# Kernel optimization log

Hardware: AMD Instinct MI355X
Metric: run time of the kernel (lower is better)

The kernel has to match this reference:

```python
import jax, jax.numpy as jnp
import numpy as np

N_QUBITS = 5
Q_DEPTH = 1
HALF_PI = np.pi / 2.0

H_GATE = (1.0 / np.sqrt(2.0)) * jnp.array([[1, 1], [1, -1]], dtype=jnp.complex64)
CNOT = jnp.array([[1, 0, 0, 0],
                  [0, 1, 0, 0],
                  [0, 0, 0, 1],
                  [0, 0, 1, 0]], dtype=jnp.complex64).reshape(2, 2, 2, 2)


def _apply_1q(state, gate, wire):
    # state: (2,)*N_QUBITS complex, gate: (2,2) complex
    state = jnp.tensordot(gate, state, axes=([1], [wire]))
    return jnp.moveaxis(state, 0, wire)


def _apply_cnot(state, control, target):
    state = jnp.tensordot(CNOT, state, axes=([2, 3], [control, target]))
    return jnp.moveaxis(state, (0, 1), (control, target))


def _ry(t):
    c = jnp.cos(t / 2).astype(jnp.complex64)
    s = jnp.sin(t / 2).astype(jnp.complex64)
    return jnp.stack([jnp.stack([c, -s]), jnp.stack([s, c])])


def _rx(t):
    c = jnp.cos(t / 2).astype(jnp.complex64)
    js = (-1j) * jnp.sin(t / 2).astype(jnp.complex64)
    return jnp.stack([jnp.stack([c, js]), jnp.stack([js, c])])


def _circuit(angles, q_weights):
    # angles: (N_QUBITS,), q_weights: (Q_DEPTH, N_QUBITS)
    state = jnp.zeros((2,) * N_QUBITS, dtype=jnp.complex64).at[(0,) * N_QUBITS].set(1.0)
    for w in range(N_QUBITS):
        state = _apply_1q(state, H_GATE, w)
    for w in range(N_QUBITS):
        state = _apply_1q(state, _ry(angles[w]), w)
    for k in range(Q_DEPTH):
        # BasicEntanglerLayers: RX rotations then ring of CNOTs
        for w in range(N_QUBITS):
            state = _apply_1q(state, _rx(q_weights[k, w]), w)
        for w in range(N_QUBITS):
            state = _apply_cnot(state, w, (w + 1) % N_QUBITS)
    probs = state.real ** 2 + state.imag ** 2
    zvals = []
    for w in range(N_QUBITS):
        p = probs.sum(axis=tuple(i for i in range(N_QUBITS) if i != w))  # (2,)
        zvals.append(p[0] - p[1])
    return jnp.stack(zvals)  # (N_QUBITS,)


def setup_inputs() -> dict:
    key = jax.random.key(0)
    k1, k2, k3, k4, k5, k6 = jax.random.split(key, 6)
    B = 65536
    return {
        "input_features": jax.random.normal(k1, (B, 512), dtype=jnp.float32),
        "w_pre": jax.random.normal(k2, (N_QUBITS, 512), dtype=jnp.float32) * 0.04,
        "b_pre": jax.random.normal(k3, (N_QUBITS,), dtype=jnp.float32) * 0.04,
        "q_params": 0.01 * jax.random.uniform(k4, (Q_DEPTH * N_QUBITS,), dtype=jnp.float32),
        "w_post": jax.random.normal(k5, (2, N_QUBITS), dtype=jnp.float32) * 0.4,
        "b_post": jax.random.normal(k6, (2,), dtype=jnp.float32) * 0.4,
    }


def reference(input_features, w_pre, b_pre, q_params, w_post, b_post):
    pre_out = input_features @ w_pre.T + b_pre            # (B, 5)
    q_in = jnp.tanh(pre_out) * HALF_PI                    # (B, 5)
    q_weights = q_params.reshape(Q_DEPTH, N_QUBITS)
    q_out = jax.vmap(lambda a: _circuit(a, q_weights))(q_in)  # (B, 5) real
    q_out = q_out.astype(jnp.float32)
    return q_out @ w_post.T + b_post                      # (B, 2)
```

## Files before the change

kernel.cpp:

```cpp
#include <hip/hip_runtime.h>
#include <math.h>

#define NQ 5
#define D 512
#define HALF_PI 1.57079632679489662f


__global__ __launch_bounds__(256) void dressed_qnet_kernel(
    const float* __restrict__ x,
    const float* __restrict__ w_pre,
    const float* __restrict__ b_pre,
    const float* __restrict__ q_params,
    const float* __restrict__ w_post,
    const float* __restrict__ b_post,
    float* __restrict__ out,
    int B)
{
    const int lane = threadIdx.x & 63;
    const int wave_in_block = threadIdx.x >> 6;
    const int waves_per_block = blockDim.x >> 6;
    const int wave_id = blockIdx.x * waves_per_block + wave_in_block;
    const int n_waves = gridDim.x * waves_per_block;

    float4 w0[NQ], w1[NQ];
#pragma unroll
    for (int q = 0; q < NQ; ++q) {
        w0[q] = *reinterpret_cast<const float4*>(w_pre + q * D + lane * 4);
        w1[q] = *reinterpret_cast<const float4*>(w_pre + q * D + 256 + lane * 4);
    }

    float bp[NQ], ct[NQ];
#pragma unroll
    for (int q = 0; q < NQ; ++q) {
        bp[q] = b_pre[q];
        ct[q] = __cosf(q_params[q]);
    }
    float wp0[NQ], wp1[NQ];
#pragma unroll
    for (int q = 0; q < NQ; ++q) {
        wp0[q] = w_post[q];
        wp1[q] = w_post[NQ + q];
    }
    const float bpost0 = b_post[0];
    const float bpost1 = b_post[1];

    for (int row = wave_id; row < B; row += n_waves) {
        const float4* xr = reinterpret_cast<const float4*>(x + (size_t)row * D);
        const float4 x0 = xr[lane];
        const float4 x1 = xr[lane + 64];

        float acc[NQ];
#pragma unroll
        for (int q = 0; q < NQ; ++q) {
            float s;
            s  = x0.x * w0[q].x;
            s  = fmaf(x0.y, w0[q].y, s);
            s  = fmaf(x0.z, w0[q].z, s);
            s  = fmaf(x0.w, w0[q].w, s);
            s  = fmaf(x1.x, w1[q].x, s);
            s  = fmaf(x1.y, w1[q].y, s);
            s  = fmaf(x1.z, w1[q].z, s);
            s  = fmaf(x1.w, w1[q].w, s);
            acc[q] = s;
        }

#pragma unroll
        for (int q = 0; q < NQ; ++q) {
            float v = acc[q];
#pragma unroll
            for (int off = 32; off >= 1; off >>= 1)
                v += __shfl_xor(v, off, 64);
            acc[q] = v;
        }

        float z[NQ];
#pragma unroll
        for (int q = 0; q < NQ; ++q) {
            const float p = acc[q] + bp[q];
            const float e = __expf(2.0f * p);
            const float th = 1.0f - 2.0f / (e + 1.0f);
            z[q] = -__sinf(HALF_PI * th) * ct[q];
        }

        const float v1   = z[0] * z[1];
        const float z234 = z[2] * z[3] * z[4];
        const float v0   = z[1] * z234;
        const float v2   = v1 * z[2];
        const float v3   = v2 * z[3];
        const float v4   = v1 * z234;

        float o0 = bpost0, o1 = bpost1;
        o0 = fmaf(wp0[0], v0, o0); o1 = fmaf(wp1[0], v0, o1);
        o0 = fmaf(wp0[1], v1, o0); o1 = fmaf(wp1[1], v1, o1);
        o0 = fmaf(wp0[2], v2, o0); o1 = fmaf(wp1[2], v2, o1);
        o0 = fmaf(wp0[3], v3, o0); o1 = fmaf(wp1[3], v3, o1);
        o0 = fmaf(wp0[4], v4, o0); o1 = fmaf(wp1[4], v4, o1);

        if (lane == 0) {
            reinterpret_cast<float2*>(out)[row] = make_float2(o0, o1);
        }
    }
}

extern "C" void kernel_launch(void* const* d_in, const int* in_sizes, int n_in,
                              void* d_out, int out_size, void* d_ws, size_t ws_size,
                              hipStream_t stream) {
    const float* x        = (const float*)d_in[0];
    const float* w_pre    = (const float*)d_in[1];
    const float* b_pre    = (const float*)d_in[2];
    const float* q_params = (const float*)d_in[3];
    const float* w_post   = (const float*)d_in[4];
    const float* b_post   = (const float*)d_in[5];
    float* out = (float*)d_out;

    const int B = in_sizes[0] / D;

    const int threads = 256;
    const int blocks = 2048;
    dressed_qnet_kernel<<<blocks, threads, 0, stream>>>(
        x, w_pre, b_pre, q_params, w_post, b_post, out, B);
}
```

Measured before the change: 33.07 us.

## Batch four rows per wave with upfront nontemporal loads and DPP wave reductions

Replaces the grid-stride row loop with a one-shot mapping in which each wave processes four rows. All of that wave's x loads are issued up front as nontemporal loads to raise memory-level parallelism. The shuffle-based wave reduction is replaced with DPP adds, a ds_swizzle and readlanes, and the four rows' outputs are written as two vector stores. The trade-off is more blocks and extra registers per wave, and the grid becomes fully sized to B.

```diff
diff --git a/kernel.cpp b/kernel.cpp
--- a/kernel.cpp
+++ b/kernel.cpp
@@ -3,8 +3,28 @@
 
 #define NQ 5
 #define D 512
+#define R 4
 #define HALF_PI 1.57079632679489662f
 
+typedef float f32x4 __attribute__((ext_vector_type(4)));
+
+
+#define DPP_ADD(v, CTRL)                                                        \
+    ((v) + __builtin_bit_cast(float, __builtin_amdgcn_update_dpp(               \
+               0, __builtin_bit_cast(int, (v)), (CTRL), 0xF, 0xF, true)))
+
+__device__ __forceinline__ float wave_sum(float v) {
+    v = DPP_ADD(v, 0xB1);
+    v = DPP_ADD(v, 0x4E);
+    v = DPP_ADD(v, 0x141);
+    v = DPP_ADD(v, 0x140);
+    int vi = __builtin_amdgcn_ds_swizzle(__builtin_bit_cast(int, v), 0x401F);
+    v = v + __builtin_bit_cast(float, vi);
+    const int vb = __builtin_bit_cast(int, v);
+    const float lo = __builtin_bit_cast(float, __builtin_amdgcn_readlane(vb, 0));
+    const float hi = __builtin_bit_cast(float, __builtin_amdgcn_readlane(vb, 32));
+    return lo + hi;
+}
 
 __global__ __launch_bounds__(256) void dressed_qnet_kernel(
     const float* __restrict__ x,
@@ -17,71 +37,72 @@
     int B)
 {
     const int lane = threadIdx.x & 63;
-    const int wave_in_block = threadIdx.x >> 6;
-    const int waves_per_block = blockDim.x >> 6;
-    const int wave_id = blockIdx.x * waves_per_block + wave_in_block;
-    const int n_waves = gridDim.x * waves_per_block;
+    const int wave = (blockIdx.x * blockDim.x + threadIdx.x) >> 6;
+    const int row0 = wave * R;
+    if (row0 >= B) return;
 
-    float4 w0[NQ], w1[NQ];
+    f32x4 xa[R], xb[R];
+#pragma unroll
+    for (int r = 0; r < R; ++r) {
+        const int row = (row0 + r < B) ? (row0 + r) : (B - 1);
+        const f32x4* xr = reinterpret_cast<const f32x4*>(x + (size_t)row * D);
+        xa[r] = __builtin_nontemporal_load(xr + lane);
+        xb[r] = __builtin_nontemporal_load(xr + lane + 64);
+    }
+
+    f32x4 w0[NQ], w1[NQ];
 #pragma unroll
     for (int q = 0; q < NQ; ++q) {
-        w0[q] = *reinterpret_cast<const float4*>(w_pre + q * D + lane * 4);
-        w1[q] = *reinterpret_cast<const float4*>(w_pre + q * D + 256 + lane * 4);
+        w0[q] = *reinterpret_cast<const f32x4*>(w_pre + q * D + lane * 4);
+        w1[q] = *reinterpret_cast<const f32x4*>(w_pre + q * D + 256 + lane * 4);
     }
 
-    float bp[NQ], ct[NQ];
+    float bp[NQ], ct[NQ], wp0[NQ], wp1[NQ];
 #pragma unroll
     for (int q = 0; q < NQ; ++q) {
-        bp[q] = b_pre[q];
-        ct[q] = __cosf(q_params[q]);
-    }
-    float wp0[NQ], wp1[NQ];
-#pragma unroll
-    for (int q = 0; q < NQ; ++q) {
+        bp[q]  = b_pre[q];
+        ct[q]  = __cosf(q_params[q]);
         wp0[q] = w_post[q];
         wp1[q] = w_post[NQ + q];
     }
     const float bpost0 = b_post[0];
     const float bpost1 = b_post[1];
 
-    for (int row = wave_id; row < B; row += n_waves) {
-        const float4* xr = reinterpret_cast<const float4*>(x + (size_t)row * D);
-        const float4 x0 = xr[lane];
-        const float4 x1 = xr[lane + 64];
-
-        float acc[NQ];
+    float acc[R][NQ];
+#pragma unroll
+    for (int r = 0; r < R; ++r) {
 #pragma unroll
         for (int q = 0; q < NQ; ++q) {
             float s;
-            s  = x0.x * w0[q].x;
-            s  = fmaf(x0.y, w0[q].y, s);
-            s  = fmaf(x0.z, w0[q].z, s);
-            s  = fmaf(x0.w, w0[q].w, s);
-            s  = fmaf(x1.x, w1[q].x, s);
-            s  = fmaf(x1.y, w1[q].y, s);
-            s  = fmaf(x1.z, w1[q].z, s);
-            s  = fmaf(x1.w, w1[q].w, s);
-            acc[q] = s;
+            s = xa[r].x * w0[q].x;
+            s = fmaf(xa[r].y, w0[q].y, s);
+            s = fmaf(xa[r].z, w0[q].z, s);
+            s = fmaf(xa[r].w, w0[q].w, s);
+            s = fmaf(xb[r].x, w1[q].x, s);
+            s = fmaf(xb[r].y, w1[q].y, s);
+            s = fmaf(xb[r].z, w1[q].z, s);
+            s = fmaf(xb[r].w, w1[q].w, s);
+            acc[r][q] = s;
         }
+    }
 
 #pragma unroll
-        for (int q = 0; q < NQ; ++q) {
-            float v = acc[q];
+    for (int r = 0; r < R; ++r)
 #pragma unroll
-            for (int off = 32; off >= 1; off >>= 1)
-                v += __shfl_xor(v, off, 64);
-            acc[q] = v;
-        }
+        for (int q = 0; q < NQ; ++q)
+            acc[r][q] = wave_sum(acc[r][q]);
 
+    float o[R][2];
+#pragma unroll
+    for (int r = 0; r < R; ++r) {
         float z[NQ];
 #pragma unroll
         for (int q = 0; q < NQ; ++q) {
-            const float p = acc[q] + bp[q];
+            const float p = acc[r][q] + bp[q];
             const float e = __expf(2.0f * p);
             const float th = 1.0f - 2.0f / (e + 1.0f);
             z[q] = -__sinf(HALF_PI * th) * ct[q];
         }
-
         const float v1   = z[0] * z[1];
         const float z234 = z[2] * z[3] * z[4];
         const float v0   = z[1] * z234;
@@ -95,9 +116,23 @@
         o0 = fmaf(wp0[2], v2, o0); o1 = fmaf(wp1[2], v2, o1);
         o0 = fmaf(wp0[3], v3, o0); o1 = fmaf(wp1[3], v3, o1);
         o0 = fmaf(wp0[4], v4, o0); o1 = fmaf(wp1[4], v4, o1);
+        o[r][0] = o0; o[r][1] = o1;
+    }
 
-        if (lane == 0) {
-            reinterpret_cast<float2*>(out)[row] = make_float2(o0, o1);
+    if (lane == 0) {
+        if (row0 + R <= B) {
+            f32x4* dst = reinterpret_cast<f32x4*>(out + (size_t)row0 * 2);
+            f32x4 d0 = { o[0][0], o[0][1], o[1][0], o[1][1] };
+            f32x4 d1 = { o[2][0], o[2][1], o[3][0], o[3][1] };
+            dst[0] = d0;
+            dst[1] = d1;
+        } else {
+#pragma unroll
+            for (int r = 0; r < R; ++r)
+                if (row0 + r < B) {
+                    out[(size_t)(row0 + r) * 2 + 0] = o[r][0];
+                    out[(size_t)(row0 + r) * 2 + 1] = o[r][1];
+                }
         }
     }
 }
@@ -116,7 +151,8 @@
     const int B = in_sizes[0] / D;
 
     const int threads = 256;
-    const int blocks = 2048;
+    const int rows_per_block = (threads / 64) * R;
+    const int blocks = (B + rows_per_block - 1) / rows_per_block;
     dressed_qnet_kernel<<<blocks, threads, 0, stream>>>(
         x, w_pre, b_pre, q_params, w_post, b_post, out, B);
 }
```

Result: slower. 34.57 us (+4.5%).
